# Kernel tuning notes

Measured on AMD Instinct MI355X. Metric: run time of the kernel, lower is better.

The kernel has to match this reference:

```python
import jax, jax.numpy as jnp
import numpy as np

N_NODES = 100000
N_EDGES = 600000
EMB = 128
L = 5
NUM_ATOM = 119
NUM_CHIR = 3
NUM_BTYPE = 5
NUM_BDIR = 3
BN_EPS = 1e-5


def setup_inputs() -> dict:
    key = jax.random.key(0)
    ks = jax.random.split(key, 16)
    inp = {}
    inp['x'] = jax.random.randint(ks[0], (N_NODES, 2), 0, NUM_ATOM, dtype=jnp.int64 if jax.config.jax_enable_x64 else jnp.int32)
    inp['edge_index'] = jax.random.randint(ks[1], (2, N_EDGES), 0, N_NODES)
    inp['edge_attr'] = jax.random.randint(ks[2], (N_EDGES, 2), 0, NUM_BDIR)
    s = 0.05
    inp['x_emb1'] = jax.random.normal(ks[3], (NUM_ATOM, EMB), jnp.float32) * s
    inp['x_emb2'] = jax.random.normal(ks[4], (NUM_CHIR, EMB), jnp.float32) * s
    inp['edge_emb1'] = jax.random.normal(ks[5], (L, NUM_BTYPE, EMB), jnp.float32) * s
    inp['edge_emb2'] = jax.random.normal(ks[6], (L, NUM_BDIR, EMB), jnp.float32) * s
    inp['W1'] = jax.random.normal(ks[7], (L, EMB, 2 * EMB), jnp.float32) * (1.0 / np.sqrt(EMB))
    inp['b1'] = jnp.zeros((L, 2 * EMB), jnp.float32)
    inp['W2'] = jax.random.normal(ks[8], (L, 2 * EMB, EMB), jnp.float32) * (1.0 / np.sqrt(2 * EMB))
    inp['b2'] = jnp.zeros((L, EMB), jnp.float32)
    inp['eps'] = jnp.zeros((L,), jnp.float32)
    inp['gamma'] = jnp.ones((L, EMB), jnp.float32)
    inp['beta'] = jnp.zeros((L, EMB), jnp.float32)
    return inp


def reference(x, edge_index, edge_attr, x_emb1, x_emb2, edge_emb1, edge_emb2,
              W1, b1, W2, b2, eps, gamma, beta):
    N = x.shape[0]
    # node embedding: sum of two table lookups
    x0 = jnp.clip(x[:, 0], 0, x_emb1.shape[0] - 1)
    x1 = jnp.clip(x[:, 1], 0, x_emb2.shape[0] - 1)
    h = x_emb1[x0] + x_emb2[x1]  # [N, EMB]
    # add self loops (loop edge_attr = zeros -> bond type 0 / dir 0)
    loop = jnp.arange(N, dtype=edge_index.dtype)
    src = jnp.concatenate([edge_index[0], loop])  # [E+N]
    dst = jnp.concatenate([edge_index[1], loop])
    ea = jnp.concatenate([edge_attr, jnp.zeros((N, 2), dtype=edge_attr.dtype)], axis=0)
    e0 = jnp.clip(ea[:, 0], 0, edge_emb1.shape[1] - 1)
    e1 = jnp.clip(ea[:, 1], 0, edge_emb2.shape[1] - 1)
    n_layers = eps.shape[0]
    for i in range(n_layers):
        e = edge_emb1[i][e0] + edge_emb2[i][e1]              # [E+N, EMB]
        m = jax.nn.relu(h[src] + e)                           # gather + elementwise
        agg = jax.ops.segment_sum(m, dst, num_segments=N)     # scatter-add
        out = (1.0 + eps[i]) * h + agg
        # MLP: Linear -> ReLU -> Linear
        hmid = jax.nn.relu(out @ W1[i] + b1[i])
        h = hmid @ W2[i] + b2[i]
        # BatchNorm1d over nodes (batch statistics, biased variance)
        mean = jnp.mean(h, axis=0)
        var = jnp.mean((h - mean) ** 2, axis=0)
        h = (h - mean) * jax.lax.rsqrt(var + BN_EPS) * gamma[i] + beta[i]
        if i < n_layers - 1:
            h = jax.nn.relu(h)
    return h
```

## Files before the change

kernel.cpp:

```cpp
#include <hip/hip_runtime.h>

#define NN 100000
#define NPAD 100096
#define NE 600000
#define EMB 128

typedef unsigned short u16;
typedef unsigned int u32;
typedef unsigned long long u64;
typedef _Float16 half8 __attribute__((ext_vector_type(8)));
typedef float f32x4 __attribute__((ext_vector_type(4)));

__device__ __forceinline__ float4 ld4(const float* p) { return *(const float4*)p; }
__device__ __forceinline__ u32 packh2(float a, float b) {
  union { _Float16 h[2]; u32 d; } u;
  u.h[0] = (_Float16)a;
  u.h[1] = (_Float16)b;
  return u.d;
}

__global__ __launch_bounds__(256) void node_init_kernel(
    const int* __restrict__ x, const float* __restrict__ emb1,
    const float* __restrict__ emb2, _Float16* __restrict__ hb) {
  int tid = blockIdx.x * blockDim.x + threadIdx.x;
  int n = tid >> 4;
  if (n >= NN) return;
  int kc = tid & 15;
  int x0 = min(max(x[2 * n], 0), 118);
  int x1 = min(max(x[2 * n + 1], 0), 2);
  const float* p1 = emb1 + (size_t)x0 * EMB + kc * 8;
  const float* p2 = emb2 + (size_t)x1 * EMB + kc * 8;
  _Float16 o[8];
#pragma unroll
  for (int j = 0; j < 8; ++j) o[j] = (_Float16)(p1[j] + p2[j]);
  *(ulonglong2*)(hb + (size_t)n * EMB + kc * 8) = *(ulonglong2*)o;
}

__global__ __launch_bounds__(256) void hist_kernel(const int* __restrict__ ei,
                                                   int* __restrict__ deg) {
  int e = blockIdx.x * blockDim.x + threadIdx.x;
  if (e >= NE) return;
  atomicAdd(&deg[ei[NE + e]], 1);
}

__global__ __launch_bounds__(256) void scan1_kernel(const int* __restrict__ deg,
                                                    int* __restrict__ off,
                                                    int* __restrict__ bsum) {
  __shared__ int s[256];
  int t = threadIdx.x;
  int base = blockIdx.x * 1024 + t * 4;
  int v[4];
#pragma unroll
  for (int j = 0; j < 4; ++j) {
    int idx = base + j;
    v[j] = (idx < NN) ? deg[idx] : 0;
  }
  int tsum = v[0] + v[1] + v[2] + v[3];
  s[t] = tsum;
  __syncthreads();
  for (int d = 1; d < 256; d <<= 1) {
    int add = (t >= d) ? s[t - d] : 0;
    __syncthreads();
    s[t] += add;
    __syncthreads();
  }
  int run = s[t] - tsum;
#pragma unroll
  for (int j = 0; j < 4; ++j) {
    int idx = base + j;
    if (idx < NN) off[idx] = run;
    run += v[j];
  }
  if (t == 255) bsum[blockIdx.x] = s[255];
}

__global__ void scan2_kernel(int* __restrict__ bsum, int* __restrict__ off, int nb) {
  if (threadIdx.x == 0) {
    int run = 0;
    for (int b = 0; b < nb; ++b) {
      int v = bsum[b];
      bsum[b] = run;
      run += v;
    }
    off[NN] = run;
  }
}

__global__ __launch_bounds__(256) void scan3_kernel(int* __restrict__ off,
                                                    const int* __restrict__ bsum) {
  int idx = blockIdx.x * blockDim.x + threadIdx.x;
  if (idx < NN) off[idx] += bsum[idx >> 10];
}

__global__ __launch_bounds__(256) void scatter_kernel(
    const int* __restrict__ ei, const int* __restrict__ ea,
    const int* __restrict__ off, int* __restrict__ cnt, int* __restrict__ csr) {
  int e = blockIdx.x * blockDim.x + threadIdx.x;
  if (e >= NE) return;
  int d = ei[NE + e];
  int s = ei[e];
  int a0 = min(max(ea[2 * e], 0), 4);
  int a1 = min(max(ea[2 * e + 1], 0), 2);
  int code = a0 * 3 + a1;
  int r = atomicAdd(&cnt[d], 1);
  csr[off[d] + r] = s | (code << 20);
}

__global__ __launch_bounds__(256) void combo_kernel(const float* __restrict__ ee1,
                                                    const float* __restrict__ ee2,
                                                    _Float16* __restrict__ cbh) {
  int idx = blockIdx.x * blockDim.x + threadIdx.x;
  if (idx >= 5 * 15 * 128) return;
  int l = idx / (15 * 128);
  int rem = idx % (15 * 128);
  int code = rem / 128;
  int f = rem % 128;
  cbh[idx] = (_Float16)(ee1[(l * 5 + code / 3) * 128 + f] + ee2[(l * 3 + code % 3) * 128 + f]);
}

__global__ __launch_bounds__(256) void prep_w_kernel(
    const float* __restrict__ W1g, const float* __restrict__ W2g,
    _Float16* __restrict__ W1f, _Float16* __restrict__ W2f) {
  int idx = blockIdx.x * blockDim.x + threadIdx.x;
  if (idx >= 40960) return;
  _Float16 o[8];
  if (idx < 20480) {
    int lane = idx & 63;
    int r = idx >> 6;
    int nt = r & 3, kt = (r >> 2) & 3, c = (r >> 4) & 3, l = r >> 6;
    int n = c * 64 + nt * 16 + (lane & 15);
    int kb = kt * 32 + (lane >> 4) * 8;
#pragma unroll
    for (int j = 0; j < 8; ++j) o[j] = (_Float16)W1g[((size_t)l * 128 + kb + j) * 256 + n];
    *(ulonglong2*)(W1f + (size_t)idx * 8) = *(ulonglong2*)o;
  } else {
    int i2 = idx - 20480;
    int lane = i2 & 63;
    int r = i2 >> 6;
    int nt = r & 7, ktl = (r >> 3) & 1, c = (r >> 4) & 3, l = r >> 6;
    int n = nt * 16 + (lane & 15);
    int kb = c * 64 + ktl * 32 + (lane >> 4) * 8;
#pragma unroll
    for (int j = 0; j < 8; ++j) o[j] = (_Float16)W2g[((size_t)l * 256 + kb + j) * 128 + n];
    *(ulonglong2*)(W2f + (size_t)i2 * 8) = *(ulonglong2*)o;
  }
}

template <bool NORM>
__global__ __launch_bounds__(256) void agg_kernel(
    const _Float16* __restrict__ hsrc, const float* __restrict__ scsh,
    const int* __restrict__ off, const int* __restrict__ csr,
    const _Float16* __restrict__ cbh, const float* __restrict__ epsp,
    _Float16* __restrict__ Af) {
  int tid = blockIdx.x * blockDim.x + threadIdx.x;
  int g = tid >> 4;
  int kc = tid & 15;
  float av[8] = {0.f, 0.f, 0.f, 0.f, 0.f, 0.f, 0.f, 0.f};
  float scv[8], shv[8];
  if (NORM) {
    float4 sa = ld4(scsh + kc * 8), sb = ld4(scsh + kc * 8 + 4);
    float4 ha = ld4(scsh + 128 + kc * 8), hbv = ld4(scsh + 128 + kc * 8 + 4);
    scv[0] = sa.x; scv[1] = sa.y; scv[2] = sa.z; scv[3] = sa.w;
    scv[4] = sb.x; scv[5] = sb.y; scv[6] = sb.z; scv[7] = sb.w;
    shv[0] = ha.x; shv[1] = ha.y; shv[2] = ha.z; shv[3] = ha.w;
    shv[4] = hbv.x; shv[5] = hbv.y; shv[6] = hbv.z; shv[7] = hbv.w;
  }
  if (g < NN) {
    const float eps1 = 1.0f + *epsp;
    ulonglong2 hraw = *(const ulonglong2*)(hsrc + (size_t)g * EMB + kc * 8);
    _Float16* hr = (_Float16*)&hraw;
    half8 c0 = *(const half8*)(cbh + kc * 8);
#pragma unroll
    for (int j = 0; j < 8; ++j) {
      float hv = (float)hr[j];
      if (NORM) hv = fmaxf(hv * scv[j] + shv[j], 0.f);
      av[j] = eps1 * hv + fmaxf(hv + (float)c0[j], 0.f);
    }
    int s0 = off[g], s1 = off[g + 1];
    int e = s0;
    for (; e + 3 < s1; e += 4) {
      int p0 = csr[e], p1 = csr[e + 1], p2 = csr[e + 2], p3 = csr[e + 3];
      ulonglong2 r0 = *(const ulonglong2*)(hsrc + (size_t)(p0 & 0xFFFFF) * EMB + kc * 8);
      ulonglong2 r1 = *(const ulonglong2*)(hsrc + (size_t)(p1 & 0xFFFFF) * EMB + kc * 8);
      ulonglong2 r2 = *(const ulonglong2*)(hsrc + (size_t)(p2 & 0xFFFFF) * EMB + kc * 8);
      ulonglong2 r3 = *(const ulonglong2*)(hsrc + (size_t)(p3 & 0xFFFFF) * EMB + kc * 8);
      ulonglong2 rr[4] = {r0, r1, r2, r3};
      int pp[4] = {p0, p1, p2, p3};
#pragma unroll
      for (int u = 0; u < 4; ++u) {
        half8 cc = *(const half8*)(cbh + (size_t)(pp[u] >> 20) * EMB + kc * 8);
        _Float16* sp = (_Float16*)&rr[u];
#pragma unroll
        for (int j = 0; j < 8; ++j) {
          float v = (float)sp[j];
          if (NORM) v = fmaxf(v * scv[j] + shv[j], 0.f);
          av[j] += fmaxf(v + (float)cc[j], 0.f);
        }
      }
    }
    for (; e < s1; ++e) {
      int p0 = csr[e];
      ulonglong2 r0 = *(const ulonglong2*)(hsrc + (size_t)(p0 & 0xFFFFF) * EMB + kc * 8);
      half8 cc = *(const half8*)(cbh + (size_t)(p0 >> 20) * EMB + kc * 8);
      _Float16* sp = (_Float16*)&r0;
#pragma unroll
      for (int j = 0; j < 8; ++j) {
        float v = (float)sp[j];
        if (NORM) v = fmaxf(v * scv[j] + shv[j], 0.f);
        av[j] += fmaxf(v + (float)cc[j], 0.f);
      }
    }
  }
  _Float16 o[8];
#pragma unroll
  for (int j = 0; j < 8; ++j) o[j] = (_Float16)av[j];
  *(ulonglong2*)(Af + (size_t)g * EMB + kc * 8) = *(ulonglong2*)o;
}

__global__ __launch_bounds__(256, 4) void mlp_kernel(
    const _Float16* __restrict__ Af, const _Float16* __restrict__ W1f,
    const _Float16* __restrict__ W2f,
    const float* __restrict__ b1g, const float* __restrict__ b2g,
    _Float16* __restrict__ hpre, float* __restrict__ slots) {
  __shared__ __align__(16) _Float16 Ws[16 * 64 * 8];

  const int t = threadIdx.x;
  const int w = t >> 6;
  const int lane = t & 63;
  const int q = lane >> 4, l15 = lane & 15;
  const int gw = blockIdx.x * 4 + w;
  const int n0 = gw * 16;
  float* sums = slots + (size_t)(gw & 31) * 256;

  half8 nh[4];
#pragma unroll
  for (int kt = 0; kt < 4; ++kt)
    nh[kt] = *(const half8*)(Af + (size_t)(n0 + l15) * EMB + kt * 32 + q * 8);

  f32x4 oacc[8];
#pragma unroll
  for (int a = 0; a < 8; ++a) oacc[a] = (f32x4){0.f, 0.f, 0.f, 0.f};

  const int srcA = ((q & 1) * 2) * 16 + l15;
  const int srcB = srcA + 16;
  const bool sel = (q >> 1) != 0;

  for (int c = 0; c < 4; ++c) {
    __syncthreads();
    {
      const _Float16* gb = W1f + ((size_t)(c * 16 + w * 4) * 64 + lane) * 8;
#pragma unroll
      for (int j = 0; j < 4; ++j)
        *(ulonglong2*)&Ws[(w * 4 + j) * 512 + lane * 8] =
            *(const ulonglong2*)(gb + (size_t)j * 512);
    }
    __syncthreads();

    f32x4 hacc[4];
#pragma unroll
    for (int a = 0; a < 4; ++a) hacc[a] = (f32x4){0.f, 0.f, 0.f, 0.f};
#pragma unroll
    for (int kt = 0; kt < 4; ++kt) {
#pragma unroll
      for (int colt = 0; colt < 4; ++colt) {
        half8 wh = *(const half8*)&Ws[(kt * 4 + colt) * 512 + lane * 8];
        hacc[colt] = __builtin_amdgcn_mfma_f32_16x16x32_f16(wh, nh[kt], hacc[colt], 0, 0, 0);
      }
    }
    __syncthreads();

    {
      const _Float16* gb = W2f + ((size_t)(c * 16 + w * 4) * 64 + lane) * 8;
#pragma unroll
      for (int j = 0; j < 4; ++j)
        *(ulonglong2*)&Ws[(w * 4 + j) * 512 + lane * 8] =
            *(const ulonglong2*)(gb + (size_t)j * 512);
    }

    u32 P01[4], P23[4];
#pragma unroll
    for (int colt = 0; colt < 4; ++colt) {
      float4 b1v = ld4(b1g + c * 64 + colt * 16 + q * 4);
      float v0 = fmaxf(hacc[colt][0] + b1v.x, 0.f);
      float v1 = fmaxf(hacc[colt][1] + b1v.y, 0.f);
      float v2 = fmaxf(hacc[colt][2] + b1v.z, 0.f);
      float v3 = fmaxf(hacc[colt][3] + b1v.w, 0.f);
      P01[colt] = packh2(v0, v1);
      P23[colt] = packh2(v2, v3);
    }
    __syncthreads();

#pragma unroll
    for (int ktl = 0; ktl < 2; ++ktl) {
      half8 bh;
      {
        union { u32 d[4]; half8 s; } uh;
        int c0 = 2 * ktl, c1 = 2 * ktl + 1;
        u32 a0, a1;
        a0 = (u32)__shfl((int)P01[c0], srcA); a1 = (u32)__shfl((int)P01[c1], srcA);
        uh.d[0] = sel ? a1 : a0;
        a0 = (u32)__shfl((int)P23[c0], srcA); a1 = (u32)__shfl((int)P23[c1], srcA);
        uh.d[1] = sel ? a1 : a0;
        a0 = (u32)__shfl((int)P01[c0], srcB); a1 = (u32)__shfl((int)P01[c1], srcB);
        uh.d[2] = sel ? a1 : a0;
        a0 = (u32)__shfl((int)P23[c0], srcB); a1 = (u32)__shfl((int)P23[c1], srcB);
        uh.d[3] = sel ? a1 : a0;
        bh = uh.s;
      }
#pragma unroll
      for (int nt = 0; nt < 8; ++nt) {
        half8 wh = *(const half8*)&Ws[(ktl * 8 + nt) * 512 + lane * 8];
        oacc[nt] = __builtin_amdgcn_mfma_f32_16x16x32_f16(wh, bh, oacc[nt], 0, 0, 0);
      }
    }
  }

  const int node = n0 + l15;
#pragma unroll
  for (int nt = 0; nt < 8; ++nt) {
    int ocb = nt * 16 + q * 4;
    float4 b2v = ld4(b2g + ocb);
    f32x4 s = (f32x4){0.f, 0.f, 0.f, 0.f};
    f32x4 s2 = (f32x4){0.f, 0.f, 0.f, 0.f};
    if (node < NN) {
      float v0 = oacc[nt][0] + b2v.x;
      float v1 = oacc[nt][1] + b2v.y;
      float v2 = oacc[nt][2] + b2v.z;
      float v3 = oacc[nt][3] + b2v.w;
      u64 pk = (u64)packh2(v0, v1) | ((u64)packh2(v2, v3) << 32);
      *(u64*)(hpre + (size_t)node * EMB + ocb) = pk;
      s[0] = v0; s[1] = v1; s[2] = v2; s[3] = v3;
      s2[0] = v0 * v0; s2[1] = v1 * v1; s2[2] = v2 * v2; s2[3] = v3 * v3;
    }
#pragma unroll
    for (int d = 1; d < 16; d <<= 1) {
#pragma unroll
      for (int r = 0; r < 4; ++r) {
        s[r] += __shfl_xor(s[r], d);
        s2[r] += __shfl_xor(s2[r], d);
      }
    }
    if (l15 == 0) {
#pragma unroll
      for (int r = 0; r < 4; ++r) {
        atomicAdd(&sums[ocb + r], s[r]);
        atomicAdd(&sums[128 + ocb + r], s2[r]);
      }
    }
  }
}

__global__ void stats_kernel(const float* __restrict__ slots,
                             const float* __restrict__ gamma,
                             const float* __restrict__ beta,
                             float* __restrict__ scsh) {
  int f = threadIdx.x;
  float s = 0.f, s2 = 0.f;
#pragma unroll 8
  for (int k = 0; k < 32; ++k) {
    s += slots[k * 256 + f];
    s2 += slots[k * 256 + 128 + f];
  }
  float mean = s * (1.0f / NN);
  float var = s2 * (1.0f / NN) - mean * mean;
  float sc = gamma[f] * rsqrtf(var + 1e-5f);
  scsh[f] = sc;
  scsh[128 + f] = beta[f] - mean * sc;
}

__global__ __launch_bounds__(256) void out_kernel(
    const _Float16* __restrict__ hpre, const float* __restrict__ scsh,
    float* __restrict__ out) {
  int tid = blockIdx.x * blockDim.x + threadIdx.x;
  int n = tid >> 4;
  if (n >= NN) return;
  int kc = tid & 15;
  ulonglong2 raw = *(const ulonglong2*)(hpre + (size_t)n * EMB + kc * 8);
  _Float16* hr = (_Float16*)&raw;
  float4 sa = ld4(scsh + kc * 8), sb = ld4(scsh + kc * 8 + 4);
  float4 ha = ld4(scsh + 128 + kc * 8), hbv = ld4(scsh + 128 + kc * 8 + 4);
  float scv[8] = {sa.x, sa.y, sa.z, sa.w, sb.x, sb.y, sb.z, sb.w};
  float shv[8] = {ha.x, ha.y, ha.z, ha.w, hbv.x, hbv.y, hbv.z, hbv.w};
  float v[8];
#pragma unroll
  for (int j = 0; j < 8; ++j) v[j] = (float)hr[j] * scv[j] + shv[j];
  float* d = out + (size_t)n * EMB + kc * 8;
  *(float4*)d = make_float4(v[0], v[1], v[2], v[3]);
  *(float4*)(d + 4) = make_float4(v[4], v[5], v[6], v[7]);
}

extern "C" void kernel_launch(void* const* d_in, const int* in_sizes, int n_in,
                              void* d_out, int out_size, void* d_ws, size_t ws_size,
                              hipStream_t stream) {
  const int* x = (const int*)d_in[0];
  const int* ei = (const int*)d_in[1];
  const int* ea = (const int*)d_in[2];
  const float* x_emb1 = (const float*)d_in[3];
  const float* x_emb2 = (const float*)d_in[4];
  const float* ee1 = (const float*)d_in[5];
  const float* ee2 = (const float*)d_in[6];
  const float* W1 = (const float*)d_in[7];
  const float* b1 = (const float*)d_in[8];
  const float* W2 = (const float*)d_in[9];
  const float* b2 = (const float*)d_in[10];
  const float* eps = (const float*)d_in[11];
  const float* gamma = (const float*)d_in[12];
  const float* beta = (const float*)d_in[13];
  float* out = (float*)d_out;

  float* slots = (float*)d_ws;
  float* scsh = slots + 5 * 32 * 256;
  _Float16* hpre = (_Float16*)(scsh + 5 * 256);
  _Float16* Af = hpre + (size_t)NN * EMB;
  _Float16* hb = Af + (size_t)NPAD * EMB;
  _Float16* W1f = hb + (size_t)NN * EMB;
  _Float16* W2f = W1f + 5 * 32768;
  _Float16* cbh = W2f + 5 * 32768;
  int* deg = (int*)(cbh + 5 * 15 * 128 + 64);
  int* off = deg + NN;
  int* csr = off + NN + 1;
  int* bsum = csr + NE;

  const int NB_SCAN = (NN + 1023) / 1024;

  hipMemsetAsync(deg, 0, NN * sizeof(int), stream);
  hipMemsetAsync(slots, 0, 5 * 32 * 256 * sizeof(float), stream);
  hist_kernel<<<(NE + 255) / 256, 256, 0, stream>>>(ei, deg);
  scan1_kernel<<<NB_SCAN, 256, 0, stream>>>(deg, off, bsum);
  scan2_kernel<<<1, 64, 0, stream>>>(bsum, off, NB_SCAN);
  scan3_kernel<<<(NN + 255) / 256, 256, 0, stream>>>(off, bsum);
  hipMemsetAsync(deg, 0, NN * sizeof(int), stream);
  scatter_kernel<<<(NE + 255) / 256, 256, 0, stream>>>(ei, ea, off, deg, csr);
  combo_kernel<<<(5 * 15 * 128 + 255) / 256, 256, 0, stream>>>(ee1, ee2, cbh);
  prep_w_kernel<<<160, 256, 0, stream>>>(W1, W2, W1f, W2f);
  node_init_kernel<<<NN * 16 / 256 + 1, 256, 0, stream>>>(x, x_emb1, x_emb2, hb);

  const int NBLK = NPAD / 64;
  for (int i = 0; i < 5; ++i) {
    if (i == 0)
      agg_kernel<false><<<NPAD * 16 / 256, 256, 0, stream>>>(
          hb, nullptr, off, csr, cbh + (size_t)i * 15 * EMB, eps + i, Af);
    else
      agg_kernel<true><<<NPAD * 16 / 256, 256, 0, stream>>>(
          hpre, scsh + (size_t)(i - 1) * 256, off, csr,
          cbh + (size_t)i * 15 * EMB, eps + i, Af);
    mlp_kernel<<<NBLK, 256, 0, stream>>>(
        Af, W1f + (size_t)i * 32768, W2f + (size_t)i * 32768,
        b1 + (size_t)i * 256, b2 + (size_t)i * 128, hpre,
        slots + (size_t)i * 32 * 256);
    stats_kernel<<<1, 128, 0, stream>>>(slots + (size_t)i * 32 * 256,
                                        gamma + (size_t)i * EMB,
                                        beta + (size_t)i * EMB,
                                        scsh + (size_t)i * 256);
  }
  out_kernel<<<NN * 16 / 256 + 1, 256, 0, stream>>>(hpre, scsh + 4 * 256, out);
}
```

Before: 673.4 us.

## Process aggregation nodes in degree-sorted order and parallelize block-sum scan

Adds a counting sort of nodes by in-degree (histogram, scan, scatter into a permutation), and the aggregation kernel now walks nodes in descending-degree order so the 16-lane groups in a wavefront have similar edge counts. This aims to reduce divergence and load imbalance across lanes in the gather loop. The trade-off is loss of node locality: reads of h, offsets and writes to Af become scattered, and three extra setup kernels run. The serial block-sum scan is also replaced by a wave-level shuffle scan.

Result: faster. 644.1 us (-4.4%).

```diff
diff --git a/kernel.cpp b/kernel.cpp
--- a/kernel.cpp
+++ b/kernel.cpp
@@ -75,15 +75,20 @@
 }
 
 __global__ void scan2_kernel(int* __restrict__ bsum, int* __restrict__ off, int nb) {
-  if (threadIdx.x == 0) {
-    int run = 0;
-    for (int b = 0; b < nb; ++b) {
-      int v = bsum[b];
-      bsum[b] = run;
-      run += v;
-    }
-    off[NN] = run;
-  }
+  int lane = threadIdx.x;
+  int v0 = (lane < nb) ? bsum[lane] : 0;
+  int v1 = (lane + 64 < nb) ? bsum[lane + 64] : 0;
+  int s0 = v0, s1 = v1;
+  for (int d = 1; d < 64; d <<= 1) {
+    int t0 = __shfl_up(s0, d);
+    int t1 = __shfl_up(s1, d);
+    if (lane >= d) { s0 += t0; s1 += t1; }
+  }
+  int tot0 = __shfl(s0, 63);
+  int tot1 = __shfl(s1, 63);
+  if (lane < nb) bsum[lane] = s0 - v0;
+  if (lane + 64 < nb) bsum[lane + 64] = tot0 + s1 - v1;
+  if (lane == 0) off[NN] = tot0 + tot1;
 }
 
 __global__ __launch_bounds__(256) void scan3_kernel(int* __restrict__ off,
@@ -106,6 +111,48 @@
   csr[off[d] + r] = s | (code << 20);
 }
 
+__global__ __launch_bounds__(256) void dhist_kernel(const int* __restrict__ deg,
+                                                    int* __restrict__ gbins) {
+  __shared__ int l[33];
+  int t = threadIdx.x;
+  if (t < 33) l[t] = 0;
+  __syncthreads();
+  int n = blockIdx.x * 256 + t;
+  if (n < NN) atomicAdd(&l[32 - min(deg[n], 32)], 1);
+  __syncthreads();
+  if (t < 33 && l[t]) atomicAdd(&gbins[t], l[t]);
+}
+
+__global__ void dscan_kernel(int* __restrict__ gbins) {
+  int lane = threadIdx.x;
+  int v = (lane < 33) ? gbins[lane] : 0;
+  int s = v;
+  for (int d = 1; d < 64; d <<= 1) {
+    int t = __shfl_up(s, d);
+    if (lane >= d) s += t;
+  }
+  if (lane < 33) gbins[lane] = s - v;
+}
+
+__global__ __launch_bounds__(256) void dscatter_kernel(const int* __restrict__ deg,
+                                                       int* __restrict__ gbins,
+                                                       int* __restrict__ perm) {
+  __shared__ int lcnt[33], lbase[33];
+  int t = threadIdx.x;
+  if (t < 33) lcnt[t] = 0;
+  __syncthreads();
+  int n = blockIdx.x * 256 + t;
+  int b = 0, r = 0;
+  if (n < NN) {
+    b = 32 - min(deg[n], 32);
+    r = atomicAdd(&lcnt[b], 1);
+  }
+  __syncthreads();
+  if (t < 33) lbase[t] = lcnt[t] ? atomicAdd(&gbins[t], lcnt[t]) : 0;
+  __syncthreads();
+  if (n < NN) perm[lbase[b] + r] = n;
+}
+
 __global__ __launch_bounds__(256) void combo_kernel(const float* __restrict__ ee1,
                                                     const float* __restrict__ ee2,
                                                     _Float16* __restrict__ cbh) {
@@ -151,7 +198,7 @@
     const _Float16* __restrict__ hsrc, const float* __restrict__ scsh,
     const int* __restrict__ off, const int* __restrict__ csr,
     const _Float16* __restrict__ cbh, const float* __restrict__ epsp,
-    _Float16* __restrict__ Af) {
+    const int* __restrict__ perm, _Float16* __restrict__ Af) {
   int tid = blockIdx.x * blockDim.x + threadIdx.x;
   int g = tid >> 4;
   int kc = tid & 15;
@@ -165,9 +212,11 @@
     shv[0] = ha.x; shv[1] = ha.y; shv[2] = ha.z; shv[3] = ha.w;
     shv[4] = hbv.x; shv[5] = hbv.y; shv[6] = hbv.z; shv[7] = hbv.w;
   }
+  int node = g;
   if (g < NN) {
+    node = perm[g];
     const float eps1 = 1.0f + *epsp;
-    ulonglong2 hraw = *(const ulonglong2*)(hsrc + (size_t)g * EMB + kc * 8);
+    ulonglong2 hraw = *(const ulonglong2*)(hsrc + (size_t)node * EMB + kc * 8);
     _Float16* hr = (_Float16*)&hraw;
     half8 c0 = *(const half8*)(cbh + kc * 8);
 #pragma unroll
@@ -176,7 +225,7 @@
       if (NORM) hv = fmaxf(hv * scv[j] + shv[j], 0.f);
       av[j] = eps1 * hv + fmaxf(hv + (float)c0[j], 0.f);
     }
-    int s0 = off[g], s1 = off[g + 1];
+    int s0 = off[node], s1 = off[node + 1];
     int e = s0;
     for (; e + 3 < s1; e += 4) {
       int p0 = csr[e], p1 = csr[e + 1], p2 = csr[e + 2], p3 = csr[e + 3];
@@ -214,7 +263,7 @@
   _Float16 o[8];
 #pragma unroll
   for (int j = 0; j < 8; ++j) o[j] = (_Float16)av[j];
-  *(ulonglong2*)(Af + (size_t)g * EMB + kc * 8) = *(ulonglong2*)o;
+  *(ulonglong2*)(Af + (size_t)node * EMB + kc * 8) = *(ulonglong2*)o;
 }
 
 __global__ __launch_bounds__(256, 4) void mlp_kernel(
@@ -420,12 +469,18 @@
   int* off = deg + NN;
   int* csr = off + NN + 1;
   int* bsum = csr + NE;
+  int* gbins = bsum + 128;
+  int* perm = gbins + 64;
 
   const int NB_SCAN = (NN + 1023) / 1024;
 
   hipMemsetAsync(deg, 0, NN * sizeof(int), stream);
+  hipMemsetAsync(gbins, 0, 64 * sizeof(int), stream);
   hipMemsetAsync(slots, 0, 5 * 32 * 256 * sizeof(float), stream);
   hist_kernel<<<(NE + 255) / 256, 256, 0, stream>>>(ei, deg);
+  dhist_kernel<<<(NN + 255) / 256, 256, 0, stream>>>(deg, gbins);
+  dscan_kernel<<<1, 64, 0, stream>>>(gbins);
+  dscatter_kernel<<<(NN + 255) / 256, 256, 0, stream>>>(deg, gbins, perm);
   scan1_kernel<<<NB_SCAN, 256, 0, stream>>>(deg, off, bsum);
   scan2_kernel<<<1, 64, 0, stream>>>(bsum, off, NB_SCAN);
   scan3_kernel<<<(NN + 255) / 256, 256, 0, stream>>>(off, bsum);
@@ -439,11 +494,11 @@
   for (int i = 0; i < 5; ++i) {
     if (i == 0)
       agg_kernel<false><<<NPAD * 16 / 256, 256, 0, stream>>>(
-          hb, nullptr, off, csr, cbh + (size_t)i * 15 * EMB, eps + i, Af);
+          hb, nullptr, off, csr, cbh + (size_t)i * 15 * EMB, eps + i, perm, Af);
     else
       agg_kernel<true><<<NPAD * 16 / 256, 256, 0, stream>>>(
           hpre, scsh + (size_t)(i - 1) * 256, off, csr,
-          cbh + (size_t)i * 15 * EMB, eps + i, Af);
+          cbh + (size_t)i * 15 * EMB, eps + i, perm, Af);
     mlp_kernel<<<NBLK, 256, 0, stream>>>(
         Af, W1f + (size_t)i * 32768, W2f + (size_t)i * 32768,
         b1 + (size_t)i * 256, b2 + (size_t)i * 128, hpre,
```
